# Performance work log

Measured on AMD Instinct MI355X. Metric: run time of the kernel, lower is better.

The kernel has to match this reference:

```python
import jax, jax.numpy as jnp
import numpy as np

B = 256          # batch
T = 256          # block_size (tril mask requires seq_len == 256)
E = 384          # n_embed
H = 6            # n_head
HS = E // H      # head_size = 64
EPS = 1e-5       # torch LayerNorm default


def layernorm(x, g, b):
    m = x.mean(-1, keepdims=True)
    v = x.var(-1, keepdims=True)  # population variance, matches torch LN
    return (x - m) * jax.lax.rsqrt(v + EPS) * g + b


def setup_inputs() -> dict:
    key = jax.random.key(0)
    ks = jax.random.split(key, 8)
    s = lambda i, shape: jax.random.normal(ks[i], shape, jnp.float32) * 0.02
    return {
        "x": jax.random.normal(ks[0], (B, T, E), jnp.float32),
        # per-head Q/K/V linears (bias=False) packed along output dim: [E, H*HS]
        "Wq": s(1, (E, E)), "Wk": s(2, (E, E)), "Wv": s(3, (E, E)),
        "Wo": s(4, (E, E)), "bo": jnp.zeros((E,), jnp.float32),
        "W1": s(5, (E, 4 * E)), "b1": jnp.zeros((4 * E,), jnp.float32),
        "W2": s(6, (4 * E, E)), "b2": jnp.zeros((E,), jnp.float32),
        "g1": jnp.ones((E,), jnp.float32), "be1": jnp.zeros((E,), jnp.float32),
        "g2": jnp.ones((E,), jnp.float32), "be2": jnp.zeros((E,), jnp.float32),
    }


def reference(x, Wq, Wk, Wv, Wo, bo, W1, b1, W2, b2, g1, be1, g2, be2):
    # Block.forward: ffwd(ln2(sa(ln1(x)) + x)) + x   (dropout = identity at eval)
    h = layernorm(x, g1, be1)                                  # [B,T,E]
    q = (h @ Wq).reshape(B, T, H, HS)
    k = (h @ Wk).reshape(B, T, H, HS)
    v = (h @ Wv).reshape(B, T, H, HS)
    wei = jnp.einsum('bqhd,bkhd->bhqk', q, k) * (HS ** -0.5)   # [B,H,T,T]
    mask = jnp.tril(jnp.ones((T, T), dtype=bool))
    wei = jnp.where(mask, wei, -jnp.inf)
    wei = jax.nn.softmax(wei, axis=-1)
    attn = jnp.einsum('bhqk,bkhd->bqhd', wei, v).reshape(B, T, E)
    sa = attn @ Wo + bo                                        # output projection
    y = sa + x                                                 # residual 1
    h2 = layernorm(y, g2, be2)
    ff = jax.nn.relu(h2 @ W1 + b1) @ W2 + b2                   # FFN
    return ff + x                                              # residual 2 (to x!)
```

## Files before the change

kernel.cpp:

```cpp
#include <hip/hip_runtime.h>
#include <hip/hip_bf16.h>

typedef unsigned short bfu;
typedef __attribute__((ext_vector_type(8))) short short8;
typedef __attribute__((ext_vector_type(4))) float f32x4;

__device__ __forceinline__ bfu f2bf(float f) {
  return __builtin_bit_cast(bfu, __float2bfloat16(f));
}

__device__ __forceinline__ void gld16(const void* g, void* l) {
  __builtin_amdgcn_global_load_lds(
      (const __attribute__((address_space(1))) void*)g,
      (__attribute__((address_space(3))) void*)l, 16, 0, 0);
}

__global__ void transpose_w(const float* __restrict__ W, bfu* __restrict__ WT,
                            int K, int N) {
  int idx = blockIdx.x * 256 + threadIdx.x;
  if (idx >= K * N) return;
  int k = idx / N, n = idx - k * N;
  WT[(size_t)n * K + k] = f2bf(W[idx]);
}

__launch_bounds__(256)
__global__ void ln_kernel(const float* __restrict__ in, const float* __restrict__ g,
                          const float* __restrict__ be, bfu* __restrict__ out) {
  const int wv = threadIdx.x >> 6, ln = threadIdx.x & 63;
  const size_t row = (size_t)blockIdx.x * 4 + wv;
  const float* p = in + row * 384;
  float v[6], s = 0.f, ss = 0.f;
#pragma unroll
  for (int i = 0; i < 6; i++) { v[i] = p[i * 64 + ln]; s += v[i]; ss += v[i] * v[i]; }
#pragma unroll
  for (int m = 1; m < 64; m <<= 1) { s += __shfl_xor(s, m); ss += __shfl_xor(ss, m); }
  const float mean = s * (1.f / 384.f);
  const float rs = rsqrtf(ss * (1.f / 384.f) - mean * mean + 1e-5f);
  bfu* q = out + row * 384;
#pragma unroll
  for (int i = 0; i < 6; i++) {
    const int c = i * 64 + ln;
    q[c] = f2bf((v[i] - mean) * rs * g[c] + be[c]);
  }
}

template <int BIAS, int RELU, int OUTBF>
__launch_bounds__(256)
__global__ void gemm_kernel(const bfu* __restrict__ A, const bfu* __restrict__ Bt,
                            const float* __restrict__ bias,
                            void* __restrict__ Cout, int N, int K, int ntn) {
  __shared__ bfu a_sm[2][128 * 32];
  __shared__ bfu b_sm[2][128 * 32];
  const int tid = threadIdx.x;
  const int wv = tid >> 6, ln = tid & 63;
  const int cpx = gridDim.x >> 3;
  const int wg = (blockIdx.x & 7) * cpx + (blockIdx.x >> 3);
  const int bm = wg / ntn, bn = wg - bm * ntn;
  const int m0 = bm << 7, n0 = bn << 7;
  const int wr = wv >> 1, wc = wv & 1;
  const int fr = ln & 15, fc = (ln >> 4) << 3;

  f32x4 acc[4][4];
#pragma unroll
  for (int i = 0; i < 4; i++)
#pragma unroll
    for (int j = 0; j < 4; j++) acc[i][j] = f32x4{0.f, 0.f, 0.f, 0.f};

  auto stage = [&](int buf, int kt) {
#pragma unroll
    for (int i = 0; i < 2; ++i) {
      const int c = wv * 2 + i;
      const int r = (c << 4) + (ln >> 2);
      const int col = kt * 32 + ((ln & 3) << 3);
      gld16(A  + (size_t)(m0 + r) * K + col, (char*)a_sm[buf] + c * 1024);
      gld16(Bt + (size_t)(n0 + r) * K + col, (char*)b_sm[buf] + c * 1024);
    }
  };

  stage(0, 0);
  __syncthreads();
  const int nk = K >> 5;
  for (int kt = 0; kt < nk; ++kt) {
    const int cur = kt & 1;
    if (kt + 1 < nk) stage(cur ^ 1, kt + 1);
    short8 af[4], bfr[4];
#pragma unroll
    for (int mi = 0; mi < 4; mi++)
      af[mi] = *(const short8*)&a_sm[cur][(wr * 64 + mi * 16 + fr) * 32 + fc];
#pragma unroll
    for (int ni = 0; ni < 4; ni++)
      bfr[ni] = *(const short8*)&b_sm[cur][(wc * 64 + ni * 16 + fr) * 32 + fc];
#pragma unroll
    for (int mi = 0; mi < 4; mi++)
#pragma unroll
      for (int ni = 0; ni < 4; ni++)
        acc[mi][ni] = __builtin_amdgcn_mfma_f32_16x16x32_bf16(af[mi], bfr[ni], acc[mi][ni], 0, 0, 0);
    __syncthreads();
  }

#pragma unroll
  for (int mi = 0; mi < 4; mi++) {
#pragma unroll
    for (int ni = 0; ni < 4; ni++) {
      const int row = m0 + wr * 64 + mi * 16 + ((ln >> 4) << 2);
      const int col = n0 + wc * 64 + ni * 16 + fr;
      float bv = 0.f;
      if (BIAS) bv = bias[col];
#pragma unroll
      for (int r = 0; r < 4; r++) {
        float v = acc[mi][ni][r] + bv;
        if (RELU) v = fmaxf(v, 0.f);
        const size_t idx = (size_t)(row + r) * N + col;
        if (OUTBF) ((bfu*)Cout)[idx] = f2bf(v);
        else       ((float*)Cout)[idx] = v;
      }
    }
  }
}

template <int LN>
__launch_bounds__(512)
__global__ void row_gemm(const bfu* __restrict__ A, const bfu* __restrict__ Bt,
                         const float* __restrict__ bias, const float* __restrict__ res,
                         const float* __restrict__ g, const float* __restrict__ be,
                         void* __restrict__ Cout, int K) {
  __shared__ bfu a_sm[2][128 * 32];
  __shared__ bfu b_sm[2][384 * 32];
  __shared__ float lnp[4][128][2];
  const int tid = threadIdx.x;
  const int wv = tid >> 6, ln = tid & 63;
  const int wr = wv >> 2, wc = wv & 3;
  const int fr = ln & 15, fc = (ln >> 4) << 3;
  const int m0 = blockIdx.x << 7;

  f32x4 acc[4][6];
#pragma unroll
  for (int i = 0; i < 4; i++)
#pragma unroll
    for (int j = 0; j < 6; j++) acc[i][j] = f32x4{0.f, 0.f, 0.f, 0.f};

  auto stage = [&](int buf, int kt) {
#pragma unroll
    for (int i = 0; i < 4; ++i) {
      const int c = wv * 4 + i;
      const int rr = (ln >> 2);
      const int col = kt * 32 + ((ln & 3) << 3);
      if (c < 8)
        gld16(A + (size_t)(m0 + (c << 4) + rr) * K + col, (char*)a_sm[buf] + c * 1024);
      else
        gld16(Bt + (size_t)(((c - 8) << 4) + rr) * K + col, (char*)b_sm[buf] + (c - 8) * 1024);
    }
  };

  stage(0, 0);
  __syncthreads();
  const int nk = K >> 5;
  for (int kt = 0; kt < nk; ++kt) {
    const int cur = kt & 1;
    if (kt + 1 < nk) stage(cur ^ 1, kt + 1);
    short8 af[4], bfr[6];
#pragma unroll
    for (int mi = 0; mi < 4; mi++)
      af[mi] = *(const short8*)&a_sm[cur][(wr * 64 + mi * 16 + fr) * 32 + fc];
#pragma unroll
    for (int ni = 0; ni < 6; ni++)
      bfr[ni] = *(const short8*)&b_sm[cur][(wc * 96 + ni * 16 + fr) * 32 + fc];
#pragma unroll
    for (int mi = 0; mi < 4; mi++)
#pragma unroll
      for (int ni = 0; ni < 6; ni++)
        acc[mi][ni] = __builtin_amdgcn_mfma_f32_16x16x32_bf16(af[mi], bfr[ni], acc[mi][ni], 0, 0, 0);
    __syncthreads();
  }

  const int rq = (ln >> 4) << 2;
#pragma unroll
  for (int mi = 0; mi < 4; mi++) {
    const int row = wr * 64 + mi * 16 + rq;
#pragma unroll
    for (int ni = 0; ni < 6; ni++) {
      const int col = wc * 96 + ni * 16 + fr;
      const float bv = bias[col];
#pragma unroll
      for (int r = 0; r < 4; r++)
        acc[mi][ni][r] += bv + res[(size_t)(m0 + row + r) * 384 + col];
    }
  }

  if (LN) {
#pragma unroll
    for (int mi = 0; mi < 4; mi++) {
      float s[4] = {0.f, 0.f, 0.f, 0.f}, ss[4] = {0.f, 0.f, 0.f, 0.f};
#pragma unroll
      for (int ni = 0; ni < 6; ni++)
#pragma unroll
        for (int r = 0; r < 4; r++) {
          const float v = acc[mi][ni][r];
          s[r] += v; ss[r] += v * v;
        }
#pragma unroll
      for (int m = 1; m < 16; m <<= 1)
#pragma unroll
        for (int r = 0; r < 4; r++) {
          s[r] += __shfl_xor(s[r], m);
          ss[r] += __shfl_xor(ss[r], m);
        }
      if (fr == 0) {
#pragma unroll
        for (int r = 0; r < 4; r++) {
          lnp[wc][wr * 64 + mi * 16 + rq + r][0] = s[r];
          lnp[wc][wr * 64 + mi * 16 + rq + r][1] = ss[r];
        }
      }
    }
    __syncthreads();
#pragma unroll
    for (int mi = 0; mi < 4; mi++) {
#pragma unroll
      for (int r = 0; r < 4; r++) {
        const int row = wr * 64 + mi * 16 + rq + r;
        const float sm = lnp[0][row][0] + lnp[1][row][0] + lnp[2][row][0] + lnp[3][row][0];
        const float sq = lnp[0][row][1] + lnp[1][row][1] + lnp[2][row][1] + lnp[3][row][1];
        const float mean = sm * (1.f / 384.f);
        const float rs = rsqrtf(sq * (1.f / 384.f) - mean * mean + 1e-5f);
#pragma unroll
        for (int ni = 0; ni < 6; ni++) {
          const int col = wc * 96 + ni * 16 + fr;
          ((bfu*)Cout)[(size_t)(m0 + row) * 384 + col] =
              f2bf((acc[mi][ni][r] - mean) * rs * g[col] + be[col]);
        }
      }
    }
  } else {
#pragma unroll
    for (int mi = 0; mi < 4; mi++) {
      const int row = wr * 64 + mi * 16 + rq;
#pragma unroll
      for (int ni = 0; ni < 6; ni++) {
        const int col = wc * 96 + ni * 16 + fr;
#pragma unroll
        for (int r = 0; r < 4; r++)
          ((float*)Cout)[(size_t)(m0 + row + r) * 384 + col] = acc[mi][ni][r];
      }
    }
  }
}

#define KPAD 72
#define VPAD 264
#define PPAD 264

__launch_bounds__(512)
__global__ void attn_kernel(const bfu* __restrict__ qkv, bfu* __restrict__ ob) {
  __shared__ bfu k_sm[256 * KPAD];
  __shared__ bfu vt_sm[64 * VPAD];
  __shared__ bfu p_sm[8 * 16 * PPAD];
  const int b = blockIdx.x / 6, h = blockIdx.x - b * 6;
  const int tid = threadIdx.x;
  const int wv = tid >> 6, ln = tid & 63;
  const int fr = ln & 15, fc = (ln >> 4) << 3;
  const size_t inbase = (size_t)b * 256 * 1152 + h * 64;
  const bfu* qb = qkv + inbase;
  const bfu* kb = qkv + inbase + 384;
  const bfu* vb = qkv + inbase + 768;
  const size_t obase = (size_t)b * 256 * 384 + h * 64;

  {
    const int row = tid >> 1;
    const int dh = (tid & 1) << 5;
    const bfu* kg = kb + (size_t)row * 1152 + dh;
    const bfu* vg = vb + (size_t)row * 1152 + dh;
#pragma unroll
    for (int i = 0; i < 4; i++) {
      short8 t8 = *(const short8*)(kg + i * 8);
      *(short8*)&k_sm[row * KPAD + dh + i * 8] = t8;
      short8 v8 = *(const short8*)(vg + i * 8);
#pragma unroll
      for (int j = 0; j < 8; j++)
        vt_sm[(dh + i * 8 + j) * VPAD + row] = (bfu)v8[j];
    }
  }
  __syncthreads();

  bfu* pw = &p_sm[wv * 16 * PPAD];
  const int rq = (ln >> 4) << 2;

#pragma unroll
  for (int si = 0; si < 2; ++si) {
    const int s = si ? (15 - wv) : wv;
    const int qr0 = s << 4;
    const int nf = s + 1;
    short8 aq[2];
#pragma unroll
    for (int dc = 0; dc < 2; dc++)
      aq[dc] = *(const short8*)(qb + (size_t)(qr0 + fr) * 1152 + dc * 32 + fc);

    f32x4 sacc[16];
#pragma unroll
    for (int f = 0; f < 16; f++) sacc[f] = f32x4{0.f, 0.f, 0.f, 0.f};
#pragma unroll
    for (int f = 0; f < 16; f++) if (f < nf) {
#pragma unroll
      for (int dc = 0; dc < 2; dc++) {
        short8 kf = *(const short8*)&k_sm[(f * 16 + fr) * KPAD + dc * 32 + fc];
        sacc[f] = __builtin_amdgcn_mfma_f32_16x16x32_bf16(aq[dc], kf, sacc[f], 0, 0, 0);
      }
    }
    float mr[4] = {-3e38f, -3e38f, -3e38f, -3e38f};
#pragma unroll
    for (int f = 0; f < 16; f++) if (f < nf) {
#pragma unroll
      for (int r = 0; r < 4; r++) {
        float sv = sacc[f][r] * 0.125f;
        if (f * 16 + fr > qr0 + rq + r) sv = -3e38f;
        sacc[f][r] = sv;
        mr[r] = fmaxf(mr[r], sv);
      }
    }
#pragma unroll
    for (int msk = 1; msk < 16; msk <<= 1) {
#pragma unroll
      for (int r = 0; r < 4; r++) mr[r] = fmaxf(mr[r], __shfl_xor(mr[r], msk));
    }
    float ls[4] = {0.f, 0.f, 0.f, 0.f};
#pragma unroll
    for (int f = 0; f < 16; f++) if (f < nf) {
#pragma unroll
      for (int r = 0; r < 4; r++) {
        float p = __expf(sacc[f][r] - mr[r]);
        sacc[f][r] = p;
        ls[r] += p;
      }
    }
#pragma unroll
    for (int msk = 1; msk < 16; msk <<= 1) {
#pragma unroll
      for (int r = 0; r < 4; r++) ls[r] += __shfl_xor(ls[r], msk);
    }
#pragma unroll
    for (int f = 0; f < 16; f++) if (f < nf) {
#pragma unroll
      for (int r = 0; r < 4; r++)
        pw[(rq + r) * PPAD + f * 16 + fr] = f2bf(sacc[f][r]);
    }
    if (nf & 1) {
#pragma unroll
      for (int r = 0; r < 4; r++) pw[(rq + r) * PPAD + nf * 16 + fr] = 0;
    }
    f32x4 oc[4];
#pragma unroll
    for (int n = 0; n < 4; n++) oc[n] = f32x4{0.f, 0.f, 0.f, 0.f};
    const int kcs = (nf + 1) >> 1;
#pragma unroll
    for (int kc = 0; kc < 8; ++kc) if (kc < kcs) {
      short8 pa = *(const short8*)&pw[fr * PPAD + kc * 32 + fc];
#pragma unroll
      for (int n = 0; n < 4; n++) {
        short8 vf = *(const short8*)&vt_sm[(n * 16 + fr) * VPAD + kc * 32 + fc];
        oc[n] = __builtin_amdgcn_mfma_f32_16x16x32_bf16(pa, vf, oc[n], 0, 0, 0);
      }
    }
    float inv[4];
#pragma unroll
    for (int r = 0; r < 4; r++) inv[r] = 1.f / ls[r];
#pragma unroll
    for (int n = 0; n < 4; n++) {
#pragma unroll
      for (int r = 0; r < 4; r++)
        ob[obase + (size_t)(qr0 + rq + r) * 384 + n * 16 + fr] = f2bf(oc[n][r] * inv[r]);
    }
  }
}

extern "C" void kernel_launch(void* const* d_in, const int* in_sizes, int n_in,
                              void* d_out, int out_size, void* d_ws, size_t ws_size,
                              hipStream_t stream) {
  const float* x   = (const float*)d_in[0];
  const float* Wq  = (const float*)d_in[1];
  const float* Wk  = (const float*)d_in[2];
  const float* Wv  = (const float*)d_in[3];
  const float* Wo  = (const float*)d_in[4];
  const float* bo  = (const float*)d_in[5];
  const float* W1  = (const float*)d_in[6];
  const float* b1  = (const float*)d_in[7];
  const float* W2  = (const float*)d_in[8];
  const float* b2  = (const float*)d_in[9];
  const float* g1  = (const float*)d_in[10];
  const float* be1 = (const float*)d_in[11];
  const float* g2  = (const float*)d_in[12];
  const float* be2 = (const float*)d_in[13];
  float* out = (float*)d_out;
  char* ws = (char*)d_ws;

  bfu* wqkvT = (bfu*)(ws + 0);
  bfu* woT   = (bfu*)(ws + 884736);
  bfu* w1T   = (bfu*)(ws + 1179648);
  bfu* w2T   = (bfu*)(ws + 2359296);
  char* H    = ws + 3538944;
  char* BIG  = H + 50331648;
  bfu* hb    = (bfu*)BIG;
  bfu* qkvb  = (bfu*)(BIG + 50331648);
  bfu* attnb = (bfu*)BIG;
  bfu* h2b   = (bfu*)H;
  bfu* ab    = (bfu*)BIG;

  transpose_w<<<576, 256, 0, stream>>>(Wq, wqkvT, 384, 384);
  transpose_w<<<576, 256, 0, stream>>>(Wk, wqkvT + 384 * 384, 384, 384);
  transpose_w<<<576, 256, 0, stream>>>(Wv, wqkvT + 2 * 384 * 384, 384, 384);
  transpose_w<<<576, 256, 0, stream>>>(Wo, woT, 384, 384);
  transpose_w<<<2304, 256, 0, stream>>>(W1, w1T, 384, 1536);
  transpose_w<<<2304, 256, 0, stream>>>(W2, w2T, 1536, 384);

  ln_kernel<<<16384, 256, 0, stream>>>(x, g1, be1, hb);

  gemm_kernel<0, 0, 1><<<4608, 256, 0, stream>>>(hb, wqkvT, nullptr, qkvb, 1152, 384, 9);

  attn_kernel<<<1536, 512, 0, stream>>>(qkvb, attnb);

  row_gemm<1><<<512, 512, 0, stream>>>(attnb, woT, bo, x, g2, be2, h2b, 384);

  gemm_kernel<1, 1, 1><<<6144, 256, 0, stream>>>(h2b, w1T, b1, ab, 1536, 384, 12);

  row_gemm<0><<<512, 512, 0, stream>>>(ab, w2T, b2, x, nullptr, nullptr, out, 1536);
}
```

Before: 537.8 us.

## Deepen GEMM LDS pipelines to triple/quad buffering with vmcnt-based waits

Both GEMM kernels now use deeper multi-buffered LDS staging: three buffers in gemm_kernel and four in row_gemm. Loads are issued two or three k-tiles ahead. The per-iteration double __syncthreads is replaced by one s_waitcnt vmcnt(N) plus a single s_barrier, so global-to-LDS loads stay in flight across several MFMA iterations and memory latency is hidden. The cost is much more LDS per block in row_gemm (about 128KB), which may reduce occupancy. Correctness also depends on the hand-counted vmcnt values matching the number of outstanding loads.

```diff
diff --git a/kernel.cpp b/kernel.cpp
--- a/kernel.cpp
+++ b/kernel.cpp
@@ -49,8 +49,8 @@
 __global__ void gemm_kernel(const bfu* __restrict__ A, const bfu* __restrict__ Bt,
                             const float* __restrict__ bias,
                             void* __restrict__ Cout, int N, int K, int ntn) {
-  __shared__ bfu a_sm[2][128 * 32];
-  __shared__ bfu b_sm[2][128 * 32];
+  __shared__ bfu a_sm[3][128 * 32];
+  __shared__ bfu b_sm[3][128 * 32];
   const int tid = threadIdx.x;
   const int wv = tid >> 6, ln = tid & 63;
   const int cpx = gridDim.x >> 3;
@@ -77,25 +77,33 @@
     }
   };
 
+  const int nk = K >> 5;
   stage(0, 0);
-  __syncthreads();
-  const int nk = K >> 5;
+  if (nk > 1) stage(1, 1);
+
+  int cb = 0;
   for (int kt = 0; kt < nk; ++kt) {
-    const int cur = kt & 1;
-    if (kt + 1 < nk) stage(cur ^ 1, kt + 1);
+    if (kt + 1 < nk) asm volatile("s_waitcnt vmcnt(4)" ::: "memory");
+    else             asm volatile("s_waitcnt vmcnt(0)" ::: "memory");
+    __builtin_amdgcn_s_barrier();
+    __builtin_amdgcn_sched_barrier(0);
+    if (kt + 2 < nk) {
+      int sb = cb + 2; if (sb >= 3) sb -= 3;
+      stage(sb, kt + 2);
+    }
     short8 af[4], bfr[4];
 #pragma unroll
     for (int mi = 0; mi < 4; mi++)
-      af[mi] = *(const short8*)&a_sm[cur][(wr * 64 + mi * 16 + fr) * 32 + fc];
+      af[mi] = *(const short8*)&a_sm[cb][(wr * 64 + mi * 16 + fr) * 32 + fc];
 #pragma unroll
     for (int ni = 0; ni < 4; ni++)
-      bfr[ni] = *(const short8*)&b_sm[cur][(wc * 64 + ni * 16 + fr) * 32 + fc];
+      bfr[ni] = *(const short8*)&b_sm[cb][(wc * 64 + ni * 16 + fr) * 32 + fc];
 #pragma unroll
     for (int mi = 0; mi < 4; mi++)
 #pragma unroll
       for (int ni = 0; ni < 4; ni++)
         acc[mi][ni] = __builtin_amdgcn_mfma_f32_16x16x32_bf16(af[mi], bfr[ni], acc[mi][ni], 0, 0, 0);
-    __syncthreads();
+    cb = (cb + 1 == 3) ? 0 : cb + 1;
   }
 
 #pragma unroll
@@ -124,8 +132,8 @@
                          const float* __restrict__ bias, const float* __restrict__ res,
                          const float* __restrict__ g, const float* __restrict__ be,
                          void* __restrict__ Cout, int K) {
-  __shared__ bfu a_sm[2][128 * 32];
-  __shared__ bfu b_sm[2][384 * 32];
+  __shared__ bfu a_sm[4][128 * 32];
+  __shared__ bfu b_sm[4][384 * 32];
   __shared__ float lnp[4][128][2];
   const int tid = threadIdx.x;
   const int wv = tid >> 6, ln = tid & 63;
@@ -152,25 +160,32 @@
     }
   };
 
-  stage(0, 0);
-  __syncthreads();
   const int nk = K >> 5;
+#pragma unroll
+  for (int i = 0; i < 3; ++i)
+    if (i < nk) stage(i, i);
+
   for (int kt = 0; kt < nk; ++kt) {
-    const int cur = kt & 1;
-    if (kt + 1 < nk) stage(cur ^ 1, kt + 1);
+    const int rem = nk - 1 - kt;
+    if (rem >= 2)      asm volatile("s_waitcnt vmcnt(8)" ::: "memory");
+    else if (rem == 1) asm volatile("s_waitcnt vmcnt(4)" ::: "memory");
+    else               asm volatile("s_waitcnt vmcnt(0)" ::: "memory");
+    __builtin_amdgcn_s_barrier();
+    __builtin_amdgcn_sched_barrier(0);
+    if (kt + 3 < nk) stage((kt + 3) & 3, kt + 3);
+    const int cb = kt & 3;
     short8 af[4], bfr[6];
 #pragma unroll
     for (int mi = 0; mi < 4; mi++)
-      af[mi] = *(const short8*)&a_sm[cur][(wr * 64 + mi * 16 + fr) * 32 + fc];
+      af[mi] = *(const short8*)&a_sm[cb][(wr * 64 + mi * 16 + fr) * 32 + fc];
 #pragma unroll
     for (int ni = 0; ni < 6; ni++)
-      bfr[ni] = *(const short8*)&b_sm[cur][(wc * 96 + ni * 16 + fr) * 32 + fc];
+      bfr[ni] = *(const short8*)&b_sm[cb][(wc * 96 + ni * 16 + fr) * 32 + fc];
 #pragma unroll
     for (int mi = 0; mi < 4; mi++)
 #pragma unroll
       for (int ni = 0; ni < 6; ni++)
         acc[mi][ni] = __builtin_amdgcn_mfma_f32_16x16x32_bf16(af[mi], bfr[ni], acc[mi][ni], 0, 0, 0);
-    __syncthreads();
   }
 
   const int rq = (ln >> 4) << 2;
```

Result: faster. 521.2 us (-3.1%).
